# Performance work log

Measured on AMD Instinct MI355X. Metric: run time of the kernel, lower is better.

The kernel has to match this reference:

```python
import jax, jax.numpy as jnp
import numpy as np

D = 768
M = 10000
B, S = 4, 2048
SCALE = 1.0 / np.sqrt(D)
LN_EPS = 1e-5


def setup_inputs() -> dict:
    key = jax.random.key(0)
    ks = jax.random.split(key, 8)
    return {
        "current_states": jax.random.normal(ks[0], (B, S, D), jnp.float32),
        "memory": jax.random.normal(ks[1], (M, D), jnp.float32),
        "gate_w": jax.random.normal(ks[2], (2 * D, 1), jnp.float32) * 0.02,
        "gate_b": jnp.zeros((1,), jnp.float32),
        "fusion_w1": jax.random.normal(ks[3], (3 * D, D), jnp.float32) * 0.02,
        "fusion_b1": jnp.zeros((D,), jnp.float32),
        "fusion_w2": jax.random.normal(ks[4], (D, D), jnp.float32) * 0.02,
        "fusion_b2": jnp.zeros((D,), jnp.float32),
        "ln_gamma": jnp.ones((D,), jnp.float32),
        "ln_beta": jnp.zeros((D,), jnp.float32),
    }


def reference(current_states, memory, gate_w, gate_b,
              fusion_w1, fusion_b1, fusion_w2, fusion_b2,
              ln_gamma, ln_beta):
    # --- MemoryBank.read: content-addressable attention over fixed memory ---
    # similarity: [B, S, M]
    sim = jnp.einsum("bsd,md->bsm", current_states, memory) * SCALE
    attn = jax.nn.softmax(sim, axis=-1)
    retrieved = jnp.einsum("bsm,md->bsd", attn, memory)  # [B, S, D]

    # --- long-term gate + residual fusion ---
    gate_in = jnp.concatenate([current_states, retrieved], axis=-1)  # [B,S,2D]
    lt_gate = jax.nn.sigmoid(gate_in @ gate_w + gate_b)  # [B,S,1]
    x = current_states + lt_gate * retrieved

    # --- memory_fusion MLP (working memory absent on first step) ---
    combined = jnp.concatenate([x, x, retrieved], axis=-1)  # [B,S,3D]
    h = jax.nn.gelu(combined @ fusion_w1 + fusion_b1, approximate=False)
    h = h @ fusion_w2 + fusion_b2

    # LayerNorm over last dim
    mu = jnp.mean(h, axis=-1, keepdims=True)
    var = jnp.var(h, axis=-1, keepdims=True)
    out = (h - mu) * jax.lax.rsqrt(var + LN_EPS) * ln_gamma + ln_beta
    return out
```

## Files before the change

kernel.cpp:

```cpp
#include <hip/hip_runtime.h>
#include <math.h>

#define N_TOK 8192
#define DIM   768
#define MEMN  10000
#define MEMP  10240
#define TQ    64
#define TM    256
#define NSPLIT 2
#define TILES_PER_SPLIT 20

constexpr float SCALE = 0.036084391824351615f;

typedef short bf16x8 __attribute__((ext_vector_type(8)));
typedef float f32x4  __attribute__((ext_vector_type(4)));

__device__ __forceinline__ unsigned short f2bf(float f) {
    unsigned u = __float_as_uint(f);
    unsigned r = (u + 0x7fffu + ((u >> 16) & 1u)) >> 16;
    return (unsigned short)r;
}

__global__ void cvt_memF(const float* __restrict__ mem, unsigned short* __restrict__ dst)
{
    const int mb = blockIdx.x;
    const bool zero = (mb >= MEMN / 16);
#pragma unroll
    for (int it = 0; it < 6; ++it) {
        const int s   = it * 256 + threadIdx.x;
        const int kc  = s >> 6;
        const int r   = s & 63;
        const int l16 = r >> 2, q = r & 3;
        unsigned short o[8];
        if (!zero) {
            const float* src = &mem[(size_t)(mb * 16 + l16) * DIM + kc * 32 + q * 8];
            float4 v0 = *(const float4*)src;
            float4 v1 = *(const float4*)(src + 4);
            o[0] = f2bf(v0.x); o[1] = f2bf(v0.y); o[2] = f2bf(v0.z); o[3] = f2bf(v0.w);
            o[4] = f2bf(v1.x); o[5] = f2bf(v1.y); o[6] = f2bf(v1.z); o[7] = f2bf(v1.w);
        } else {
#pragma unroll
            for (int j = 0; j < 8; ++j) o[j] = 0;
        }
        *(uint4*)&dst[((size_t)mb * 24 + kc) * 512 + r * 8] = *(const uint4*)o;
    }
}

__global__ void cvt_qH(const float* __restrict__ q, unsigned short* __restrict__ dst)
{
    const size_t i = ((size_t)blockIdx.x * 256 + threadIdx.x) * 4;
    float4 v = *(const float4*)&q[i];
    ushort4 o;
    o.x = f2bf(v.x); o.y = f2bf(v.y); o.z = f2bf(v.z); o.w = f2bf(v.w);
    *(ushort4*)&dst[i] = o;
}

__global__ void cvt_memS(const float* __restrict__ mem, unsigned short* __restrict__ dst)
{
    __shared__ float T[32][65];
    const int mc = blockIdx.x;
    const int d0 = blockIdx.y * 64;
    const int tx = threadIdx.x & 63;
    const int ty = threadIdx.x >> 6;
#pragma unroll
    for (int i = 0; i < 8; ++i) {
        const int row = ty + 4 * i;
        const int m   = mc * 32 + row;
        T[row][tx] = (m < MEMN) ? mem[(size_t)m * DIM + d0 + tx] : 0.f;
    }
    __syncthreads();
    const int dbl = threadIdx.x >> 6;
    const int r   = threadIdx.x & 63;
    const int l16 = r >> 2, q = r & 3;
    unsigned short o[8];
#pragma unroll
    for (int j = 0; j < 8; ++j) o[j] = f2bf(T[q * 8 + j][dbl * 16 + l16]);
    *(uint4*)&dst[((size_t)(d0 / 16 + dbl) * 320 + mc) * 512 + r * 8] = *(const uint4*)o;
}

__global__ void prep_w12T(const float* __restrict__ w1, unsigned short* __restrict__ wt)
{
    __shared__ float T[32][33];
    const int kb = blockIdx.x * 32, nb = blockIdx.y * 32;
    const int tx = threadIdx.x & 31, ty = threadIdx.x >> 5;
#pragma unroll
    for (int i = 0; i < 4; ++i) {
        int k = kb + ty + 8 * i;
        float v = w1[(size_t)(768 + k) * DIM + nb + tx];
        if (kb < 768) v += w1[(size_t)k * DIM + nb + tx];
        T[ty + 8 * i][tx] = v;
    }
    __syncthreads();
    if (threadIdx.x < 128) {
        const int sub = threadIdx.x >> 6;
        const int r   = threadIdx.x & 63;
        const int l16 = r >> 2, q = r & 3;
        unsigned short o[8];
#pragma unroll
        for (int j = 0; j < 8; ++j) o[j] = f2bf(T[q * 8 + j][sub * 16 + l16]);
        const int n16 = (nb >> 4) + sub;
        const int kc  = kb >> 5;
        *(uint4*)&wt[((size_t)n16 * 48 + kc) * 512 + r * 8] = *(const uint4*)o;
    }
}

__global__ void prep_w2T(const float* __restrict__ w2, unsigned short* __restrict__ wt)
{
    __shared__ float T[32][33];
    const int kb = blockIdx.x * 32, nb = blockIdx.y * 32;
    const int tx = threadIdx.x & 31, ty = threadIdx.x >> 5;
#pragma unroll
    for (int i = 0; i < 4; ++i)
        T[ty + 8 * i][tx] = w2[(size_t)(kb + ty + 8 * i) * DIM + nb + tx];
    __syncthreads();
    if (threadIdx.x < 128) {
        const int sub = threadIdx.x >> 6;
        const int r   = threadIdx.x & 63;
        const int l16 = r >> 2, q = r & 3;
        unsigned short o[8];
#pragma unroll
        for (int j = 0; j < 8; ++j) o[j] = f2bf(T[q * 8 + j][sub * 16 + l16]);
        const int n16 = (nb >> 4) + sub;
        const int kc  = kb >> 5;
        *(uint4*)&wt[((size_t)n16 * 24 + kc) * 512 + r * 8] = *(const uint4*)o;
    }
}

template <int PLAIN>
__global__ __launch_bounds__(1024, 4)
void attn_mfma(const unsigned short* __restrict__ qH, const unsigned short* __restrict__ memF,
               const unsigned short* __restrict__ memS,
               float* __restrict__ retrRaw, float* __restrict__ Lvec)
{
    __shared__ __align__(16) unsigned short Qs[64 * 768];
    __shared__ __align__(16) unsigned short Ps[64 * 256];
    __shared__ float Lred[16][64];

    const int tid    = threadIdx.x;
    const int w      = tid >> 6;
    const int lane   = tid & 63;
    const int quad   = lane >> 4;
    const int l16    = lane & 15;
    const int fr     = ((l16 << 2) | quad) << 3;

    const int split = blockIdx.y;
    const int q0    = blockIdx.x * TQ;

    const int dbase  = w * 48;
    const int mstrip = w * 16;

    {
        const int qr  = tid >> 4;
        const int db0 = tid & 15;
        const unsigned short* src = qH + (size_t)(q0 + qr) * DIM;
        const int sw = qr & 7;
#pragma unroll
        for (int i = 0; i < 6; ++i) {
            int db = db0 + i * 16;
            uint4 v = *(const uint4*)&src[db * 8];
            *(uint4*)&Qs[qr * 768 + ((db ^ sw) << 3)] = v;
        }
    }
    __syncthreads();

    f32x4 oacc[4][3];
#pragma unroll
    for (int a = 0; a < 4; ++a)
#pragma unroll
        for (int b = 0; b < 3; ++b) oacc[a][b] = (f32x4){0.f, 0.f, 0.f, 0.f};
    float lsum[4][4];
#pragma unroll
    for (int a = 0; a < 4; ++a)
#pragma unroll
        for (int r = 0; r < 4; ++r) lsum[a][r] = 0.f;

    const int xsw = l16 & 7;

    for (int st = 0; st < TILES_PER_SPLIT; ++st) {
        const int m0  = (split * TILES_PER_SPLIT + st) * TM;
        const int mc0 = m0 >> 5;

        f32x4 sacc[4];
#pragma unroll
        for (int a = 0; a < 4; ++a) sacc[a] = (f32x4){0.f, 0.f, 0.f, 0.f};

        const unsigned short* fb = memF + ((size_t)(m0 >> 4) + w) * 12288 + fr;

        bf16x8 pb[2];
        pb[0] = *(const bf16x8*)(fb);
        pb[1] = *(const bf16x8*)(fb + 512);

#pragma unroll
        for (int ks = 0; ks < 24; ++ks) {
            const int xq = (((ks << 2) + quad) ^ xsw) << 3;
            bf16x8 a0 = *(const bf16x8*)&Qs[l16 * 768 + xq];
            bf16x8 a1 = *(const bf16x8*)&Qs[(16 + l16) * 768 + xq];
            bf16x8 a2 = *(const bf16x8*)&Qs[(32 + l16) * 768 + xq];
            bf16x8 a3 = *(const bf16x8*)&Qs[(48 + l16) * 768 + xq];
            bf16x8 b = pb[ks & 1];
            sacc[0] = __builtin_amdgcn_mfma_f32_16x16x32_bf16(a0, b, sacc[0], 0, 0, 0);
            sacc[1] = __builtin_amdgcn_mfma_f32_16x16x32_bf16(a1, b, sacc[1], 0, 0, 0);
            sacc[2] = __builtin_amdgcn_mfma_f32_16x16x32_bf16(a2, b, sacc[2], 0, 0, 0);
            sacc[3] = __builtin_amdgcn_mfma_f32_16x16x32_bf16(a3, b, sacc[3], 0, 0, 0);
            if (ks < 22) pb[ks & 1] = *(const bf16x8*)(fb + (ks + 2) * 512);
        }

        __syncthreads();

        {
            const int mloc = mstrip + l16;
            const bool ok  = (m0 + mloc) < MEMN;
#pragma unroll
            for (int qt = 0; qt < 4; ++qt)
#pragma unroll
                for (int r = 0; r < 4; ++r) {
                    float p = ok ? __expf(sacc[qt][r] * SCALE) : 0.f;
                    const int q = qt * 16 + quad * 4 + r;
                    lsum[qt][r] += p;
                    Ps[q * 256 + (((mloc >> 3) ^ (q & 7)) << 3) + (mloc & 7)] = f2bf(p);
                }
        }

        __syncthreads();

        const unsigned short* msp = memS + ((size_t)(3 * w) * 320 + mc0) * 512 + fr;
        bf16x8 cb[2][3];
#pragma unroll
        for (int nt = 0; nt < 3; ++nt) {
            cb[0][nt] = *(const bf16x8*)(msp + (size_t)nt * 163840);
            cb[1][nt] = *(const bf16x8*)(msp + (size_t)nt * 163840 + 512);
        }

#pragma unroll
        for (int ks = 0; ks < 8; ++ks) {
            const int xp = (((ks << 2) + quad) ^ xsw) << 3;
            bf16x8 pa0 = *(const bf16x8*)&Ps[l16 * 256 + xp];
            bf16x8 pa1 = *(const bf16x8*)&Ps[(16 + l16) * 256 + xp];
            bf16x8 pa2 = *(const bf16x8*)&Ps[(32 + l16) * 256 + xp];
            bf16x8 pa3 = *(const bf16x8*)&Ps[(48 + l16) * 256 + xp];
            const bool dopf = (ks < 6);
#pragma unroll
            for (int nt = 0; nt < 3; ++nt) {
                oacc[0][nt] = __builtin_amdgcn_mfma_f32_16x16x32_bf16(pa0, cb[ks & 1][nt], oacc[0][nt], 0, 0, 0);
                oacc[1][nt] = __builtin_amdgcn_mfma_f32_16x16x32_bf16(pa1, cb[ks & 1][nt], oacc[1][nt], 0, 0, 0);
                oacc[2][nt] = __builtin_amdgcn_mfma_f32_16x16x32_bf16(pa2, cb[ks & 1][nt], oacc[2][nt], 0, 0, 0);
                oacc[3][nt] = __builtin_amdgcn_mfma_f32_16x16x32_bf16(pa3, cb[ks & 1][nt], oacc[3][nt], 0, 0, 0);
                if (dopf) cb[ks & 1][nt] = *(const bf16x8*)(msp + (size_t)nt * 163840 + (ks + 2) * 512);
            }
        }
    }

    float* ob = retrRaw + (PLAIN ? (size_t)split * ((size_t)N_TOK * DIM) : (size_t)0);
#pragma unroll
    for (int qt = 0; qt < 4; ++qt)
#pragma unroll
        for (int nt = 0; nt < 3; ++nt)
#pragma unroll
            for (int r = 0; r < 4; ++r) {
                const size_t idx = (size_t)(q0 + qt * 16 + quad * 4 + r) * DIM + dbase + nt * 16 + l16;
                if (PLAIN)
                    ob[idx] = oacc[qt][nt][r];
                else
                    __hip_atomic_fetch_add(&ob[idx], oacc[qt][nt][r],
                                           __ATOMIC_RELAXED, __HIP_MEMORY_SCOPE_AGENT);
            }

#pragma unroll
    for (int qt = 0; qt < 4; ++qt)
#pragma unroll
        for (int r = 0; r < 4; ++r) {
            float v = lsum[qt][r];
#pragma unroll
            for (int off = 1; off < 16; off <<= 1) v += __shfl_xor(v, off);
            if (l16 == 0) {
                if (PLAIN)
                    Lred[w][qt * 16 + quad * 4 + r] = v;
                else
                    __hip_atomic_fetch_add(&Lvec[q0 + qt * 16 + quad * 4 + r], v,
                                           __ATOMIC_RELAXED, __HIP_MEMORY_SCOPE_AGENT);
            }
        }
    if (PLAIN) {
        __syncthreads();
        if (tid < 64) {
            float s = 0.f;
#pragma unroll
            for (int ww = 0; ww < 16; ++ww) s += Lred[ww][tid];
            Lvec[(size_t)split * N_TOK + q0 + tid] = s;
        }
    }
}

template <int PLAIN>
__global__ __launch_bounds__(256)
void finalize_xr(const float* __restrict__ retrRaw, const float* __restrict__ Lvec,
                 const float* __restrict__ cs, const float* __restrict__ gw,
                 const float* __restrict__ gb, unsigned short* __restrict__ XRb)
{
    const int lane = threadIdx.x & 63;
    const int row  = blockIdx.x * 4 + (threadIdx.x >> 6);
    const float lv = PLAIN ? (Lvec[row] + Lvec[N_TOK + row]) : Lvec[row];
    const float rl = 1.0f / lv;
    const float* rr  = retrRaw + (size_t)row * DIM;
    const float* rr1 = retrRaw + (size_t)N_TOK * DIM + (size_t)row * DIM;
    const float* cr = cs + (size_t)row * DIM;

    float4 rv[3], cv[3];
    float d = 0.f;
#pragma unroll
    for (int i = 0; i < 3; ++i) {
        const int c4 = i * 256 + lane * 4;
        float4 r = *(const float4*)&rr[c4];
        if (PLAIN) {
            float4 r1 = *(const float4*)&rr1[c4];
            r.x += r1.x; r.y += r1.y; r.z += r1.z; r.w += r1.w;
        }
        r.x *= rl; r.y *= rl; r.z *= rl; r.w *= rl;
        float4 c = *(const float4*)&cr[c4];
        float4 g1 = *(const float4*)&gw[c4];
        float4 g2 = *(const float4*)&gw[DIM + c4];
        d += c.x * g1.x + c.y * g1.y + c.z * g1.z + c.w * g1.w;
        d += r.x * g2.x + r.y * g2.y + r.z * g2.z + r.w * g2.w;
        rv[i] = r; cv[i] = c;
    }
#pragma unroll
    for (int off = 32; off > 0; off >>= 1) d += __shfl_xor(d, off);
    d += gb[0];
    const float g = 1.0f / (1.0f + __expf(-d));

    unsigned short* xb = XRb + (size_t)row * 1536;
#pragma unroll
    for (int i = 0; i < 3; ++i) {
        const int c4 = i * 256 + lane * 4;
        ushort4 xo, ro;
        xo.x = f2bf(cv[i].x + g * rv[i].x); xo.y = f2bf(cv[i].y + g * rv[i].y);
        xo.z = f2bf(cv[i].z + g * rv[i].z); xo.w = f2bf(cv[i].w + g * rv[i].w);
        ro.x = f2bf(rv[i].x); ro.y = f2bf(rv[i].y);
        ro.z = f2bf(rv[i].z); ro.w = f2bf(rv[i].w);
        *(ushort4*)&xb[c4] = xo;
        *(ushort4*)&xb[DIM + c4] = ro;
    }
}

template <int K, int ACT>
__global__ __launch_bounds__(256, 2)
void gemm_mfma(const unsigned short* __restrict__ A, const unsigned short* __restrict__ WT,
               const float* __restrict__ bias, const float* __restrict__ gamma,
               const float* __restrict__ beta, void* __restrict__ outv)
{
    __shared__ __align__(16) unsigned short As[16 * 256];
    __shared__ float red[2][4][16];

    const int tid  = threadIdx.x;
    const int w    = tid >> 6;
    const int lane = tid & 63;
    const int quad = lane >> 4;
    const int l16  = lane & 15;
    const int row0 = blockIdx.x * 16;
    const int nbase = w * 192;
    const int xsw3 = l16 & 7;
    const int KC   = K / 32;
    const int fr   = ((l16 << 2) | quad) << 3;
    const int nb16 = w * 12;

    f32x4 acc[12];
#pragma unroll
    for (int nt = 0; nt < 12; ++nt) acc[nt] = (f32x4){0.f, 0.f, 0.f, 0.f};

    bf16x8 b[12];
#pragma unroll
    for (int nt = 0; nt < 12; ++nt)
        b[nt] = *(const bf16x8*)&WT[(size_t)(nb16 + nt) * KC * 512 + fr];

    for (int ch = 0; ch < K / 256; ++ch) {
        const int kc0 = ch * 256;
        __syncthreads();
#pragma unroll
        for (int i = 0; i < 2; ++i) {
            const int f = tid + i * 256;
            const int r = f >> 5, kb8 = f & 31;
            *(uint4*)&As[r * 256 + ((kb8 ^ (r & 7)) << 3)] =
                *(const uint4*)&A[(size_t)(row0 + r) * K + kc0 + kb8 * 8];
        }
        __syncthreads();
#pragma unroll
        for (int ks = 0; ks < 8; ++ks) {
            const int kc = ks * 32;
            bf16x8 af = *(const bf16x8*)&As[l16 * 256 + ((((kc >> 3) + quad) ^ xsw3) << 3)];
            int kn = ch * 8 + ks + 1;
            if (kn >= KC) kn = 0;
#pragma unroll
            for (int nt = 0; nt < 12; ++nt) {
                acc[nt] = __builtin_amdgcn_mfma_f32_16x16x32_bf16(af, b[nt], acc[nt], 0, 0, 0);
                b[nt] = *(const bf16x8*)&WT[((size_t)(nb16 + nt) * KC + kn) * 512 + fr];
            }
        }
    }

    float bv[12];
#pragma unroll
    for (int nt = 0; nt < 12; ++nt) bv[nt] = bias[nbase + nt * 16 + l16];

    if (ACT == 0) {
        unsigned short* out = (unsigned short*)outv;
#pragma unroll
        for (int nt = 0; nt < 12; ++nt)
#pragma unroll
            for (int r = 0; r < 4; ++r) {
                const int row = row0 + quad * 4 + r;
                float v = acc[nt][r] + bv[nt];
                v = 0.5f * v * (1.0f + erff(v * 0.7071067811865476f));
                out[(size_t)row * DIM + nbase + nt * 16 + l16] = f2bf(v);
            }
    } else {
        float* out = (float*)outv;
        float v[12][4];
        float s1[4] = {0.f, 0.f, 0.f, 0.f}, s2[4] = {0.f, 0.f, 0.f, 0.f};
#pragma unroll
        for (int nt = 0; nt < 12; ++nt)
#pragma unroll
            for (int r = 0; r < 4; ++r) {
                float t = acc[nt][r] + bv[nt];
                v[nt][r] = t;
                s1[r] += t;
                s2[r] += t * t;
            }
#pragma unroll
        for (int r = 0; r < 4; ++r) {
#pragma unroll
            for (int off = 1; off < 16; off <<= 1) {
                s1[r] += __shfl_xor(s1[r], off);
                s2[r] += __shfl_xor(s2[r], off);
            }
            if (l16 == 0) {
                red[0][w][quad * 4 + r] = s1[r];
                red[1][w][quad * 4 + r] = s2[r];
            }
        }
        __syncthreads();
#pragma unroll
        for (int r = 0; r < 4; ++r) {
            const int rl16 = quad * 4 + r;
            const float t1 = red[0][0][rl16] + red[0][1][rl16] + red[0][2][rl16] + red[0][3][rl16];
            const float t2 = red[1][0][rl16] + red[1][1][rl16] + red[1][2][rl16] + red[1][3][rl16];
            const float mu  = t1 * (1.0f / 768.0f);
            const float var = fmaxf(t2 * (1.0f / 768.0f) - mu * mu, 0.f);
            const float rs  = rsqrtf(var + 1e-5f);
            const int row = row0 + rl16;
#pragma unroll
            for (int nt = 0; nt < 12; ++nt) {
                const int col = nbase + nt * 16 + l16;
                out[(size_t)row * DIM + col] = (v[nt][r] - mu) * rs * gamma[col] + beta[col];
            }
        }
    }
}

extern "C" void kernel_launch(void* const* d_in, const int* in_sizes, int n_in,
                              void* d_out, int out_size, void* d_ws, size_t ws_size,
                              hipStream_t stream)
{
    const float* cs  = (const float*)d_in[0];
    const float* mem = (const float*)d_in[1];
    const float* gw  = (const float*)d_in[2];
    const float* gb  = (const float*)d_in[3];
    const float* fw1 = (const float*)d_in[4];
    const float* fb1 = (const float*)d_in[5];
    const float* fw2 = (const float*)d_in[6];
    const float* fb2 = (const float*)d_in[7];
    const float* gam = (const float*)d_in[8];
    const float* bet = (const float*)d_in[9];
    float* out = (float*)d_out;

    char* ws = (char*)d_ws;
    const size_t PLAIN_WS = 97976320;
    const bool plain = (ws_size >= PLAIN_WS);

    unsigned short* memF = (unsigned short*)ws;
    unsigned short* memS = (unsigned short*)(ws + 15728640);
    unsigned short* qH   = (unsigned short*)(ws + 31457280);
    float*          retr = (float*)(ws + 44040192);
    float*          Lvec;
    unsigned short* w12T;
    unsigned short* w2T;
    if (plain) {
        Lvec = (float*)(ws + 94371840);
        w12T = (unsigned short*)(ws + 94437376);
        w2T  = (unsigned short*)(ws + 96796672);
    } else {
        Lvec = (float*)(ws + 69206016);
        w12T = (unsigned short*)(ws + 69238784);
        w2T  = (unsigned short*)(ws + 71598080);
    }
    unsigned short* XRb  = (unsigned short*)ws;
    unsigned short* hb   = qH;

    if (!plain)
        hipMemsetAsync(retr, 0, 25165824 + 32768, stream);

    cvt_memF<<<MEMP / 16, 256, 0, stream>>>(mem, memF);
    cvt_qH<<<(N_TOK * DIM) / (256 * 4), 256, 0, stream>>>(cs, qH);
    cvt_memS<<<dim3(MEMP / 32, DIM / 64), 256, 0, stream>>>(mem, memS);
    prep_w12T<<<dim3(48, 24), 256, 0, stream>>>(fw1, w12T);
    prep_w2T<<<dim3(24, 24), 256, 0, stream>>>(fw2, w2T);

    if (plain) {
        attn_mfma<1><<<dim3(N_TOK / TQ, NSPLIT), 1024, 0, stream>>>(qH, memF, memS, retr, Lvec);
        finalize_xr<1><<<N_TOK / 4, 256, 0, stream>>>(retr, Lvec, cs, gw, gb, XRb);
    } else {
        attn_mfma<0><<<dim3(N_TOK / TQ, NSPLIT), 1024, 0, stream>>>(qH, memF, memS, retr, Lvec);
        finalize_xr<0><<<N_TOK / 4, 256, 0, stream>>>(retr, Lvec, cs, gw, gb, XRb);
    }
    gemm_mfma<1536, 0><<<N_TOK / 16, 256, 0, stream>>>(XRb, w12T, fb1, nullptr, nullptr, hb);
    gemm_mfma<768, 1><<<N_TOK / 16, 256, 0, stream>>>(hb, w2T, fb2, gam, bet, out);
}
```

Measured before the change: 937.5 us.

## Fuse gate finalize, both MLP GEMMs and LayerNorm into one tail kernel

Merges the finalize/gate kernel and the two MLP GEMM kernels into a single kernel per 16-row tile. The gated x and retrieved rows and the GELU hidden activations are kept in swizzled shared memory instead of being written to and read back from global buffers. This removes two kernel launches and the global round trips for the intermediate XR and H tensors. In exchange it uses about 72KB of LDS per block, which can lower occupancy, and all the LDS staging is done up front instead of chunk by chunk.

```diff
diff --git a/kernel.cpp b/kernel.cpp
--- a/kernel.cpp
+++ b/kernel.cpp
@@ -292,63 +292,17 @@
 }
 
 template <int PLAIN>
-__global__ __launch_bounds__(256)
-void finalize_xr(const float* __restrict__ retrRaw, const float* __restrict__ Lvec,
-                 const float* __restrict__ cs, const float* __restrict__ gw,
-                 const float* __restrict__ gb, unsigned short* __restrict__ XRb)
-{
-    const int lane = threadIdx.x & 63;
-    const int row  = blockIdx.x * 4 + (threadIdx.x >> 6);
-    const float lv = PLAIN ? (Lvec[row] + Lvec[N_TOK + row]) : Lvec[row];
-    const float rl = 1.0f / lv;
-    const float* rr  = retrRaw + (size_t)row * DIM;
-    const float* rr1 = retrRaw + (size_t)N_TOK * DIM + (size_t)row * DIM;
-    const float* cr = cs + (size_t)row * DIM;
-
-    float4 rv[3], cv[3];
-    float d = 0.f;
-#pragma unroll
-    for (int i = 0; i < 3; ++i) {
-        const int c4 = i * 256 + lane * 4;
-        float4 r = *(const float4*)&rr[c4];
-        if (PLAIN) {
-            float4 r1 = *(const float4*)&rr1[c4];
-            r.x += r1.x; r.y += r1.y; r.z += r1.z; r.w += r1.w;
-        }
-        r.x *= rl; r.y *= rl; r.z *= rl; r.w *= rl;
-        float4 c = *(const float4*)&cr[c4];
-        float4 g1 = *(const float4*)&gw[c4];
-        float4 g2 = *(const float4*)&gw[DIM + c4];
-        d += c.x * g1.x + c.y * g1.y + c.z * g1.z + c.w * g1.w;
-        d += r.x * g2.x + r.y * g2.y + r.z * g2.z + r.w * g2.w;
-        rv[i] = r; cv[i] = c;
-    }
-#pragma unroll
-    for (int off = 32; off > 0; off >>= 1) d += __shfl_xor(d, off);
-    d += gb[0];
-    const float g = 1.0f / (1.0f + __expf(-d));
-
-    unsigned short* xb = XRb + (size_t)row * 1536;
-#pragma unroll
-    for (int i = 0; i < 3; ++i) {
-        const int c4 = i * 256 + lane * 4;
-        ushort4 xo, ro;
-        xo.x = f2bf(cv[i].x + g * rv[i].x); xo.y = f2bf(cv[i].y + g * rv[i].y);
-        xo.z = f2bf(cv[i].z + g * rv[i].z); xo.w = f2bf(cv[i].w + g * rv[i].w);
-        ro.x = f2bf(rv[i].x); ro.y = f2bf(rv[i].y);
-        ro.z = f2bf(rv[i].z); ro.w = f2bf(rv[i].w);
-        *(ushort4*)&xb[c4] = xo;
-        *(ushort4*)&xb[DIM + c4] = ro;
-    }
-}
-
-template <int K, int ACT>
 __global__ __launch_bounds__(256, 2)
-void gemm_mfma(const unsigned short* __restrict__ A, const unsigned short* __restrict__ WT,
-               const float* __restrict__ bias, const float* __restrict__ gamma,
-               const float* __restrict__ beta, void* __restrict__ outv)
-{
-    __shared__ __align__(16) unsigned short As[16 * 256];
+void fused_tail(const float* __restrict__ retrRaw, const float* __restrict__ Lvec,
+                const float* __restrict__ cs, const float* __restrict__ gw,
+                const float* __restrict__ gb,
+                const unsigned short* __restrict__ W12T, const float* __restrict__ fb1,
+                const unsigned short* __restrict__ W2T,  const float* __restrict__ fb2,
+                const float* __restrict__ gamma, const float* __restrict__ beta,
+                float* __restrict__ out)
+{
+    __shared__ __align__(16) unsigned short XRl[6 * 4096];
+    __shared__ __align__(16) unsigned short Hl[3 * 4096];
     __shared__ float red[2][4][16];
 
     const int tid  = threadIdx.x;
@@ -359,10 +313,58 @@
     const int row0 = blockIdx.x * 16;
     const int nbase = w * 192;
     const int xsw3 = l16 & 7;
-    const int KC   = K / 32;
     const int fr   = ((l16 << 2) | quad) << 3;
     const int nb16 = w * 12;
 
+#pragma unroll
+    for (int it = 0; it < 4; ++it) {
+        const int rl = it * 4 + w;
+        const int row = row0 + rl;
+        const float lv = PLAIN ? (Lvec[row] + Lvec[N_TOK + row]) : Lvec[row];
+        const float rli = 1.0f / lv;
+        const float* rr  = retrRaw + (size_t)row * DIM;
+        const float* rr1 = retrRaw + (size_t)N_TOK * DIM + (size_t)row * DIM;
+        const float* cr  = cs + (size_t)row * DIM;
+
+        float4 rv[3], cv[3];
+        float d = 0.f;
+#pragma unroll
+        for (int i = 0; i < 3; ++i) {
+            const int c4 = i * 256 + lane * 4;
+            float4 r = *(const float4*)&rr[c4];
+            if (PLAIN) {
+                float4 r1 = *(const float4*)&rr1[c4];
+                r.x += r1.x; r.y += r1.y; r.z += r1.z; r.w += r1.w;
+            }
+            r.x *= rli; r.y *= rli; r.z *= rli; r.w *= rli;
+            float4 c = *(const float4*)&cr[c4];
+            float4 g1 = *(const float4*)&gw[c4];
+            float4 g2 = *(const float4*)&gw[DIM + c4];
+            d += c.x * g1.x + c.y * g1.y + c.z * g1.z + c.w * g1.w;
+            d += r.x * g2.x + r.y * g2.y + r.z * g2.z + r.w * g2.w;
+            rv[i] = r; cv[i] = c;
+        }
+#pragma unroll
+        for (int off = 32; off > 0; off >>= 1) d += __shfl_xor(d, off);
+        d += gb[0];
+        const float g = 1.0f / (1.0f + __expf(-d));
+
+        const int g8 = lane >> 1;
+        const int lo = (lane & 1) * 4;
+#pragma unroll
+        for (int i = 0; i < 3; ++i) {
+            ushort4 xo, ro;
+            xo.x = f2bf(cv[i].x + g * rv[i].x); xo.y = f2bf(cv[i].y + g * rv[i].y);
+            xo.z = f2bf(cv[i].z + g * rv[i].z); xo.w = f2bf(cv[i].w + g * rv[i].w);
+            ro.x = f2bf(rv[i].x); ro.y = f2bf(rv[i].y);
+            ro.z = f2bf(rv[i].z); ro.w = f2bf(rv[i].w);
+            const int sw = ((g8 ^ (rl & 7)) << 3) + lo;
+            *(ushort4*)&XRl[i * 4096 + rl * 256 + sw] = xo;
+            *(ushort4*)&XRl[(3 + i) * 4096 + rl * 256 + sw] = ro;
+        }
+    }
+    __syncthreads();
+
     f32x4 acc[12];
 #pragma unroll
     for (int nt = 0; nt < 12; ++nt) acc[nt] = (f32x4){0.f, 0.f, 0.f, 0.f};
@@ -370,57 +372,80 @@
     bf16x8 b[12];
 #pragma unroll
     for (int nt = 0; nt < 12; ++nt)
-        b[nt] = *(const bf16x8*)&WT[(size_t)(nb16 + nt) * KC * 512 + fr];
-
-    for (int ch = 0; ch < K / 256; ++ch) {
-        const int kc0 = ch * 256;
-        __syncthreads();
-#pragma unroll
-        for (int i = 0; i < 2; ++i) {
-            const int f = tid + i * 256;
-            const int r = f >> 5, kb8 = f & 31;
-            *(uint4*)&As[r * 256 + ((kb8 ^ (r & 7)) << 3)] =
-                *(const uint4*)&A[(size_t)(row0 + r) * K + kc0 + kb8 * 8];
-        }
-        __syncthreads();
+        b[nt] = *(const bf16x8*)&W12T[(size_t)(nb16 + nt) * 48 * 512 + fr];
+
+#pragma unroll
+    for (int ch = 0; ch < 6; ++ch) {
 #pragma unroll
         for (int ks = 0; ks < 8; ++ks) {
-            const int kc = ks * 32;
-            bf16x8 af = *(const bf16x8*)&As[l16 * 256 + ((((kc >> 3) + quad) ^ xsw3) << 3)];
+            bf16x8 af = *(const bf16x8*)&XRl[ch * 4096 + l16 * 256 + ((((ks << 2) + quad) ^ xsw3) << 3)];
             int kn = ch * 8 + ks + 1;
-            if (kn >= KC) kn = 0;
+            if (kn >= 48) kn = 0;
 #pragma unroll
             for (int nt = 0; nt < 12; ++nt) {
                 acc[nt] = __builtin_amdgcn_mfma_f32_16x16x32_bf16(af, b[nt], acc[nt], 0, 0, 0);
-                b[nt] = *(const bf16x8*)&WT[((size_t)(nb16 + nt) * KC + kn) * 512 + fr];
-            }
-        }
-    }
-
-    float bv[12];
-#pragma unroll
-    for (int nt = 0; nt < 12; ++nt) bv[nt] = bias[nbase + nt * 16 + l16];
-
-    if (ACT == 0) {
-        unsigned short* out = (unsigned short*)outv;
-#pragma unroll
-        for (int nt = 0; nt < 12; ++nt)
+                b[nt] = *(const bf16x8*)&W12T[((size_t)(nb16 + nt) * 48 + kn) * 512 + fr];
+            }
+        }
+    }
+
+    {
+        float bv[12];
+#pragma unroll
+        for (int nt = 0; nt < 12; ++nt) bv[nt] = fb1[nbase + nt * 16 + l16];
+#pragma unroll
+        for (int nt = 0; nt < 12; ++nt) {
+            const int col = nbase + nt * 16 + l16;
+            const int cch = col >> 8;
+            const int g8  = (col >> 3) & 31;
 #pragma unroll
             for (int r = 0; r < 4; ++r) {
-                const int row = row0 + quad * 4 + r;
+                const int rowl = quad * 4 + r;
                 float v = acc[nt][r] + bv[nt];
                 v = 0.5f * v * (1.0f + erff(v * 0.7071067811865476f));
-                out[(size_t)row * DIM + nbase + nt * 16 + l16] = f2bf(v);
-            }
-    } else {
-        float* out = (float*)outv;
+                Hl[cch * 4096 + rowl * 256 + ((g8 ^ (rowl & 7)) << 3) + (l16 & 7)] = f2bf(v);
+            }
+        }
+    }
+
+    bf16x8 b2[12];
+#pragma unroll
+    for (int nt = 0; nt < 12; ++nt)
+        b2[nt] = *(const bf16x8*)&W2T[(size_t)(nb16 + nt) * 24 * 512 + fr];
+
+    __syncthreads();
+
+    f32x4 acc2[12];
+#pragma unroll
+    for (int nt = 0; nt < 12; ++nt) acc2[nt] = (f32x4){0.f, 0.f, 0.f, 0.f};
+
+#pragma unroll
+    for (int ch = 0; ch < 3; ++ch) {
+#pragma unroll
+        for (int ks = 0; ks < 8; ++ks) {
+            bf16x8 af = *(const bf16x8*)&Hl[ch * 4096 + l16 * 256 + ((((ks << 2) + quad) ^ xsw3) << 3)];
+            int kn = ch * 8 + ks + 1;
+            if (kn >= 24) kn = 0;
+#pragma unroll
+            for (int nt = 0; nt < 12; ++nt) {
+                acc2[nt] = __builtin_amdgcn_mfma_f32_16x16x32_bf16(af, b2[nt], acc2[nt], 0, 0, 0);
+                b2[nt] = *(const bf16x8*)&W2T[((size_t)(nb16 + nt) * 24 + kn) * 512 + fr];
+            }
+        }
+    }
+
+    {
+        float bv[12];
+#pragma unroll
+        for (int nt = 0; nt < 12; ++nt) bv[nt] = fb2[nbase + nt * 16 + l16];
+
         float v[12][4];
         float s1[4] = {0.f, 0.f, 0.f, 0.f}, s2[4] = {0.f, 0.f, 0.f, 0.f};
 #pragma unroll
         for (int nt = 0; nt < 12; ++nt)
 #pragma unroll
             for (int r = 0; r < 4; ++r) {
-                float t = acc[nt][r] + bv[nt];
+                float t = acc2[nt][r] + bv[nt];
                 v[nt][r] = t;
                 s1[r] += t;
                 s2[r] += t * t;
@@ -492,8 +517,6 @@
         w12T = (unsigned short*)(ws + 69238784);
         w2T  = (unsigned short*)(ws + 71598080);
     }
-    unsigned short* XRb  = (unsigned short*)ws;
-    unsigned short* hb   = qH;
 
     if (!plain)
         hipMemsetAsync(retr, 0, 25165824 + 32768, stream);
@@ -506,11 +529,11 @@
 
     if (plain) {
         attn_mfma<1><<<dim3(N_TOK / TQ, NSPLIT), 1024, 0, stream>>>(qH, memF, memS, retr, Lvec);
-        finalize_xr<1><<<N_TOK / 4, 256, 0, stream>>>(retr, Lvec, cs, gw, gb, XRb);
+        fused_tail<1><<<N_TOK / 16, 256, 0, stream>>>(retr, Lvec, cs, gw, gb,
+                                                      w12T, fb1, w2T, fb2, gam, bet, out);
     } else {
         attn_mfma<0><<<dim3(N_TOK / TQ, NSPLIT), 1024, 0, stream>>>(qH, memF, memS, retr, Lvec);
-        finalize_xr<0><<<N_TOK / 4, 256, 0, stream>>>(retr, Lvec, cs, gw, gb, XRb);
-    }
-    gemm_mfma<1536, 0><<<N_TOK / 16, 256, 0, stream>>>(XRb, w12T, fb1, nullptr, nullptr, hb);
-    gemm_mfma<768, 1><<<N_TOK / 16, 256, 0, stream>>>(hb, w2T, fb2, gam, bet, out);
-}
+        fused_tail<0><<<N_TOK / 16, 256, 0, stream>>>(retr, Lvec, cs, gw, gb,
+                                                      w12T, fb1, w2T, fb2, gam, bet, out);
+    }
+}
```

Result: faster. 838.7 us (-10.5%).
